# Optimization experiments

Measured on AMD Instinct MI355X. Metric: run time of the kernel, lower is better.

The kernel has to match this reference:

```python
import jax, jax.numpy as jnp
import numpy as np

N = 524288          # batch size
NUM_SD = 64         # socio-demographic chars
H = 128             # hidden size of TasteParams MLP
NUM_ALT_FEAT = 9    # alternative features
NUM_CLASSES = 3
# utility_structure: class k -> (start, end) column slice of x
SEGMENTS = [(0, 3), (3, 6), (6, 9)]


def setup_inputs() -> dict:
    key = jax.random.key(0)
    ks = jax.random.split(key, 8)
    s = 0.05
    return {
        "x": jax.random.normal(ks[0], (N, NUM_ALT_FEAT), jnp.float32),
        "z": jax.random.normal(ks[1], (N, NUM_SD), jnp.float32),
        "W1": jax.random.normal(ks[2], (NUM_SD, H), jnp.float32) * s,
        "b1": jax.random.normal(ks[3], (H,), jnp.float32) * s,
        "W2": jax.random.normal(ks[4], (H, H), jnp.float32) * s,
        "b2": jax.random.normal(ks[5], (H,), jnp.float32) * s,
        "W3": jax.random.normal(ks[6], (H, NUM_ALT_FEAT + NUM_CLASSES), jnp.float32) * s,
        "b3": jax.random.normal(ks[7], (NUM_ALT_FEAT + NUM_CLASSES,), jnp.float32) * s,
    }


def _forward(x, z, W1, b1, W2, b2, W3, b3):
    # TasteParams MLP: Linear-ReLU-Linear-ReLU-Linear
    h = jax.nn.relu(z @ W1 + b1)
    h = jax.nn.relu(h @ W2 + b2)
    b = h @ W3 + b3                        # (N, 12)
    # monotonic_constraints (num_classes==3, func_intercept=True)
    b = jnp.concatenate([
        -jax.nn.relu(-b[:, :6]),
        b[:, 6:7],
        -jax.nn.relu(-b[:, 7:9]),
        b[:, -NUM_CLASSES:],
    ], axis=1)
    taste = b[:, :NUM_ALT_FEAT]            # (N, 9)
    intercept = b[:, -NUM_CLASSES:]        # (N, 3)
    # MNL_layer with b: per-segment elementwise mult + reduce into logits column
    prod = x * taste                       # (N, 9)
    logits = jnp.stack(
        [prod[:, lo:hi].sum(axis=1) for (lo, hi) in SEGMENTS], axis=1
    )                                      # (N, 3)
    return logits + intercept


def reference(x, z, W1, b1, W2, b2, W3, b3):
    return _forward(x, z, W1, b1, W2, b2, W3, b3)
```

## Files before the change

kernel.cpp:

```cpp
#include <hip/hip_runtime.h>
#include <hip/hip_bf16.h>


typedef __bf16 bf16x8 __attribute__((ext_vector_type(8)));
typedef float  f32x16 __attribute__((ext_vector_type(16)));
typedef unsigned int uint2v __attribute__((ext_vector_type(2)));
typedef unsigned int uint4v __attribute__((ext_vector_type(4)));

#define MFMA32(a, b, c) __builtin_amdgcn_mfma_f32_32x32x16_bf16((a), (b), (c), 0, 0, 0)
#define PIN_AGPR(v) asm("" : "+a"(v))

#define SW3 0
#define SW1 1536
#define SW2 9728
#define SB1 26112
#define SB2 26240
#define SB3 26368
#define ZS_BYTE 52768
#define SMEM_ELTS (26384 + 32768)

#define NBLK    256
#define NTHR    512
#define NTILE   16384
#define WSTRIDE (NBLK * 8)

typedef __attribute__((address_space(3))) unsigned int lds_u32;
typedef __attribute__((address_space(1))) const unsigned int glb_u32;

__device__ __forceinline__ void gll16(const float* g, const void* l) {
  __builtin_amdgcn_global_load_lds((glb_u32*)g, (lds_u32*)l, 16, 0, 0);
}

__device__ __forceinline__ unsigned pkbf(float lo, float hi) {
  unsigned short lb = __builtin_bit_cast(unsigned short, (__bf16)lo);
  unsigned short hb = __builtin_bit_cast(unsigned short, (__bf16)hi);
  return ((unsigned)hb << 16) | (unsigned)lb;
}

template <int SUB>
__device__ __forceinline__ bf16x8 mk_bfrag(const f32x16 h) {
  constexpr int B = SUB * 8;
  unsigned p01 = pkbf(h[B + 0], h[B + 1]);
  unsigned p23 = pkbf(h[B + 2], h[B + 3]);
  unsigned p45 = pkbf(h[B + 4], h[B + 5]);
  unsigned p67 = pkbf(h[B + 6], h[B + 7]);
  unsigned d0, d1, d2, d3;
#if __has_builtin(__builtin_amdgcn_permlane32_swap)
  uint2v r1 = __builtin_amdgcn_permlane32_swap(p01, p45, false, false);
  uint2v r2 = __builtin_amdgcn_permlane32_swap(p23, p67, false, false);
  d0 = r1[0]; d2 = r1[1];
  d1 = r2[0]; d3 = r2[1];
#else
  int hi = (threadIdx.x >> 5) & 1;
  unsigned sp01 = (unsigned)__shfl_xor((int)p01, 32, 64);
  unsigned sp23 = (unsigned)__shfl_xor((int)p23, 32, 64);
  unsigned sp45 = (unsigned)__shfl_xor((int)p45, 32, 64);
  unsigned sp67 = (unsigned)__shfl_xor((int)p67, 32, 64);
  d0 = hi ? sp45 : p01;
  d2 = hi ? p45  : sp01;
  d1 = hi ? sp67 : p23;
  d3 = hi ? p67  : sp23;
#endif
  uint4v t; t[0] = d0; t[1] = d1; t[2] = d2; t[3] = d3;
  return __builtin_bit_cast(bf16x8, t);
}

__device__ __forceinline__ bf16x8 ldw(const __bf16* sm, int vaddr, int imm) {
  return *(const bf16x8*)((const char*)sm + vaddr + imm);
}

__device__ __forceinline__ float4 ldz(const __bf16* sm, int vaddr) {
  return *(const float4*)((const char*)sm + vaddr);
}

__device__ __forceinline__ bf16x8 biasA(__bf16 v) {
  bf16x8 f;
  #pragma unroll
  for (int i = 0; i < 8; ++i) f[i] = (__bf16)0.0f;
  f[0] = v;
  return f;
}

__global__ __launch_bounds__(512, 2)
void tastenet_kernel(const float* __restrict__ x, const float* __restrict__ z,
                     const float* __restrict__ W1, const float* __restrict__ b1,
                     const float* __restrict__ W2, const float* __restrict__ b2,
                     const float* __restrict__ W3, const float* __restrict__ b3,
                     float* __restrict__ out) {
  __shared__ __align__(16) __bf16 sm[SMEM_ELTS];
  const int tid = threadIdx.x;
  unsigned* smw = (unsigned*)sm;

  for (int i = tid; i < 4096; i += NTHR) {
    int m = i & 127, k = (i >> 7) * 2;
    smw[SW1 / 2 + m * 32 + (((k >> 3) ^ (m & 7)) << 2) + ((k >> 1) & 3)] =
        pkbf(W1[k * 128 + m], W1[(k + 1) * 128 + m]);
  }
  for (int i = tid; i < 8192; i += NTHR) {
    int m = i & 127, k = (i >> 7) * 2;
    smw[SW2 / 2 + m * 64 + (((k >> 3) ^ (m & 7)) << 2) + ((k >> 1) & 3)] =
        pkbf(W2[k * 128 + m], W2[(k + 1) * 128 + m]);
  }
  for (int i = tid; i < 768; i += NTHR) {
    int kk = i / 12, m = i - kk * 12, k = kk * 2;
    smw[SW3 / 2 + m * 64 + (((k >> 3) ^ (m & 7)) << 2) + ((k >> 1) & 3)] =
        pkbf(W3[k * 12 + m], W3[(k + 1) * 12 + m]);
  }
  if (tid < 128) { sm[SB1 + tid] = (__bf16)b1[tid]; sm[SB2 + tid] = (__bf16)b2[tid]; }
  if (tid < 12)  sm[SB3 + tid] = (__bf16)b3[tid];
  __syncthreads();

  const int wave = tid >> 6;
  const int lane = tid & 63;
  const int q    = lane >> 5;
  const int n    = lane & 31;
  const int s8   = n & 7;
  const int eq   = q ^ (s8 & 1);
  const int sh   = s8 >> 1;

  int aw1[4], aw2[4];
  #pragma unroll
  for (int j = 0; j < 4; ++j) {
    aw1[j] = n * 128 + eq * 16 + 32 * (j ^ sh);
    aw2[j] = n * 256 + eq * 16 + 32 * (j ^ sh);
  }

  const char* slotp = (const char*)sm + ZS_BYTE + wave * 8192;
  const int lr = lane >> 4, lc = lane & 15;
  int gofs[8];
  #pragma unroll
  for (int i = 0; i < 8; ++i) {
    int r = 4 * i + lr;
    gofs[i] = r * 64 + ((lc ^ (r & 15)) << 2);
  }
  int zrd[8];
  #pragma unroll
  for (int kt = 0; kt < 4; ++kt)
    #pragma unroll
    for (int s = 0; s < 2; ++s)
      zrd[2 * kt + s] =
          ZS_BYTE + wave * 8192 + n * 256 + (((4 * kt + 2 * q + s) ^ (n & 15)) << 4);

  bf16x8 ones;
  #pragma unroll
  for (int i = 0; i < 8; ++i) ones[i] = (__bf16)0.0f;
  if (q == 0) ones[0] = (__bf16)1.0f;
  PIN_AGPR(ones);

  bf16x8 ba1[4], ba2[4], ba3;
  #pragma unroll
  for (int f = 0; f < 4; ++f) {
    ba1[f] = biasA((q == 0) ? sm[SB1 + f * 32 + n] : (__bf16)0.0f);
    ba2[f] = biasA((q == 0) ? sm[SB2 + f * 32 + n] : (__bf16)0.0f);
    PIN_AGPR(ba1[f]); PIN_AGPR(ba2[f]);
  }
  ba3 = biasA((q == 0 && n < 12) ? sm[SB3 + n] : (__bf16)0.0f);
  PIN_AGPR(ba3);

  f32x16 zeroC;
  #pragma unroll
  for (int i = 0; i < 16; ++i) zeroC[i] = 0.0f;
  PIN_AGPR(zeroC);

  const int wid = blockIdx.x * 8 + wave;

  {
    const float* zb = z + (long)wid * 2048;
    #pragma unroll
    for (int i = 0; i < 8; ++i) gll16(zb + gofs[i], slotp + (i << 10));
  }

  #pragma unroll 1
  for (int t = wid; t < NTILE; t += WSTRIDE) {
    const long row = (long)t * 32 + n;

    asm volatile("s_waitcnt vmcnt(0)" ::: "memory");

    const float* xr = x + row * 9;
    float xv0 = xr[q * 4 + 0], xv1 = xr[q * 4 + 1];
    float xv2 = xr[q * 4 + 2], xv3 = xr[q * 4 + 3];
    float xv4 = xr[8];

    bf16x8 bz[4];
    #pragma unroll
    for (int kt = 0; kt < 4; ++kt) {
      float4 a = ldz(sm, zrd[2 * kt]);
      float4 b = ldz(sm, zrd[2 * kt + 1]);
      bf16x8 f;
      f[0] = (__bf16)a.x; f[1] = (__bf16)a.y; f[2] = (__bf16)a.z; f[3] = (__bf16)a.w;
      f[4] = (__bf16)b.x; f[5] = (__bf16)b.y; f[6] = (__bf16)b.z; f[7] = (__bf16)b.w;
      bz[kt] = f;
    }
    __builtin_amdgcn_sched_barrier(0);

    if (t + WSTRIDE < NTILE) {
      const float* zb = z + (long)(t + WSTRIDE) * 2048;
      #pragma unroll
      for (int i = 0; i < 8; ++i) gll16(zb + gofs[i], slotp + (i << 10));
    }
    __builtin_amdgcn_sched_barrier(0);

    bf16x8 bf2[8];
    #pragma unroll
    for (int fp = 0; fp < 2; ++fp) {
      f32x16 aA = MFMA32(ba1[2 * fp + 0], ones, zeroC);
      f32x16 aB = MFMA32(ba1[2 * fp + 1], ones, zeroC);
      PIN_AGPR(aA); PIN_AGPR(aB);
      #pragma unroll
      for (int kt = 0; kt < 4; ++kt) {
        aA = MFMA32(ldw(sm, aw1[kt], SW1 * 2 + (2 * fp + 0) * 4096), bz[kt], aA);
        aB = MFMA32(ldw(sm, aw1[kt], SW1 * 2 + (2 * fp + 1) * 4096), bz[kt], aB);
      }
      #pragma unroll
      for (int i = 0; i < 16; ++i) { aA[i] = fmaxf(aA[i], 0.0f); aB[i] = fmaxf(aB[i], 0.0f); }
      bf2[4 * fp + 0] = mk_bfrag<0>(aA);
      bf2[4 * fp + 1] = mk_bfrag<1>(aA);
      bf2[4 * fp + 2] = mk_bfrag<0>(aB);
      bf2[4 * fp + 3] = mk_bfrag<1>(aB);
    }

    f32x16 acc3 = MFMA32(ba3, ones, zeroC);
    PIN_AGPR(acc3);
    #pragma unroll
    for (int fp = 0; fp < 2; ++fp) {
      f32x16 aA = MFMA32(ba2[2 * fp + 0], ones, zeroC);
      f32x16 aB = MFMA32(ba2[2 * fp + 1], ones, zeroC);
      PIN_AGPR(aA); PIN_AGPR(aB);
      #pragma unroll
      for (int kt = 0; kt < 8; ++kt) {
        aA = MFMA32(ldw(sm, aw2[kt & 3], SW2 * 2 + (2 * fp + 0) * 8192 + 128 * (kt >> 2)),
                    bf2[kt], aA);
        aB = MFMA32(ldw(sm, aw2[kt & 3], SW2 * 2 + (2 * fp + 1) * 8192 + 128 * (kt >> 2)),
                    bf2[kt], aB);
      }
      #pragma unroll
      for (int i = 0; i < 16; ++i) { aA[i] = fmaxf(aA[i], 0.0f); aB[i] = fmaxf(aB[i], 0.0f); }
      acc3 = MFMA32(ldw(sm, aw2[0], SW3 * 2 + 128 * fp), mk_bfrag<0>(aA), acc3);
      acc3 = MFMA32(ldw(sm, aw2[1], SW3 * 2 + 128 * fp), mk_bfrag<1>(aA), acc3);
      acc3 = MFMA32(ldw(sm, aw2[2], SW3 * 2 + 128 * fp), mk_bfrag<0>(aB), acc3);
      acc3 = MFMA32(ldw(sm, aw2[3], SW3 * 2 + 128 * fp), mk_bfrag<1>(aB), acc3);
    }

    float t0 = acc3[0], t1 = acc3[1], t2 = acc3[2], t3 = acc3[3];
    float t4 = acc3[4], t5 = acc3[5], t6 = acc3[6], t7 = acc3[7];
    float o0 = 0.f, o1 = 0.f, o2 = 0.f, g1v = 0.f, g2v = 0.f;
    if (q == 0) {
      t0 = fminf(t0, 0.0f); t1 = fminf(t1, 0.0f);
      t2 = fminf(t2, 0.0f); t3 = fminf(t3, 0.0f);
      t4 = fminf(t4, 0.0f);
      o0 = xv0 * t0 + xv1 * t1 + xv2 * t2 + t5;
      o1 = xv3 * t3 + t6;
      o2 = xv4 * t4 + t7;
    } else {
      t0 = fminf(t0, 0.0f); t1 = fminf(t1, 0.0f);
      t3 = fminf(t3, 0.0f);
      g1v = xv0 * t0 + xv1 * t1;
      g2v = xv2 * t2 + xv3 * t3;
    }
    float a1v = __shfl_xor(g1v, 32, 64);
    float a2v = __shfl_xor(g2v, 32, 64);
    if (q == 0) {
      float* op = out + row * 3;
      op[0] = o0;
      op[1] = o1 + a1v;
      op[2] = o2 + a2v;
    }
  }
}

extern "C" void kernel_launch(void* const* d_in, const int* in_sizes, int n_in,
                              void* d_out, int out_size, void* d_ws, size_t ws_size,
                              hipStream_t stream) {
  const float* x  = (const float*)d_in[0];
  const float* z  = (const float*)d_in[1];
  const float* W1 = (const float*)d_in[2];
  const float* b1 = (const float*)d_in[3];
  const float* W2 = (const float*)d_in[4];
  const float* b2 = (const float*)d_in[5];
  const float* W3 = (const float*)d_in[6];
  const float* b3 = (const float*)d_in[7];
  tastenet_kernel<<<dim3(NBLK), dim3(NTHR), 0, stream>>>(
      x, z, W1, b1, W2, b2, W3, b3, (float*)d_out);
}
```

Before: 241.1 us.

## Split each tile across a wave pair with register-resident weight fragments

```diff
diff --git a/kernel.cpp b/kernel.cpp
--- a/kernel.cpp
+++ b/kernel.cpp
@@ -16,13 +16,16 @@
 #define SB1 26112
 #define SB2 26240
 #define SB3 26368
-#define ZS_BYTE 52768
-#define SMEM_ELTS (26384 + 32768)
-
-#define NBLK    256
-#define NTHR    512
-#define NTILE   16384
-#define WSTRIDE (NBLK * 8)
+#define SMEM_ELTS 26384
+
+#define ZSL(team)  ((team) * 8192)
+#define H1X(team)  (16384 + (team) * 8192)
+#define A3X(team)  (32768 + (team) * 2048)
+
+#define NBLK 512
+#define NTHR 256
+#define NTILE 16384
+#define TSTRIDE (NBLK * 2)
 
 typedef __attribute__((address_space(3))) unsigned int lds_u32;
 typedef __attribute__((address_space(1))) const unsigned int glb_u32;
@@ -68,7 +71,6 @@
 __device__ __forceinline__ bf16x8 ldw(const __bf16* sm, int vaddr, int imm) {
   return *(const bf16x8*)((const char*)sm + vaddr + imm);
 }
-
 __device__ __forceinline__ float4 ldz(const __bf16* sm, int vaddr) {
   return *(const float4*)((const char*)sm + vaddr);
 }
@@ -81,7 +83,7 @@
   return f;
 }
 
-__global__ __launch_bounds__(512, 2)
+__global__ __launch_bounds__(256, 2)
 void tastenet_kernel(const float* __restrict__ x, const float* __restrict__ z,
                      const float* __restrict__ W1, const float* __restrict__ b1,
                      const float* __restrict__ W2, const float* __restrict__ b2,
@@ -90,6 +92,7 @@
   __shared__ __align__(16) __bf16 sm[SMEM_ELTS];
   const int tid = threadIdx.x;
   unsigned* smw = (unsigned*)sm;
+  char* smb = (char*)sm;
 
   for (int i = tid; i < 4096; i += NTHR) {
     int m = i & 127, k = (i >> 7) * 2;
@@ -117,15 +120,62 @@
   const int s8   = n & 7;
   const int eq   = q ^ (s8 & 1);
   const int sh   = s8 >> 1;
-
-  int aw1[4], aw2[4];
+  const int half = wave & 1;
+  const int team = wave >> 1;
+
+  int aw1v[4], aw2v[4];
   #pragma unroll
   for (int j = 0; j < 4; ++j) {
-    aw1[j] = n * 128 + eq * 16 + 32 * (j ^ sh);
-    aw2[j] = n * 256 + eq * 16 + 32 * (j ^ sh);
-  }
-
-  const char* slotp = (const char*)sm + ZS_BYTE + wave * 8192;
+    aw1v[j] = n * 128 + eq * 16 + 32 * (j ^ sh);
+    aw2v[j] = n * 256 + eq * 16 + 32 * (j ^ sh);
+  }
+
+  bf16x8 w1f[8], w2f[16], w3f[4];
+  #pragma unroll
+  for (int b = 0; b < 2; ++b)
+    #pragma unroll
+    for (int kt = 0; kt < 4; ++kt) {
+      w1f[b * 4 + kt] = ldw(sm, aw1v[kt] + (2 * half + b) * 4096, SW1 * 2);
+      PIN_AGPR(w1f[b * 4 + kt]);
+    }
+  #pragma unroll
+  for (int b = 0; b < 2; ++b)
+    #pragma unroll
+    for (int kt = 0; kt < 8; ++kt) {
+      w2f[b * 8 + kt] =
+          ldw(sm, aw2v[kt & 3] + (2 * half + b) * 8192 + 128 * (kt >> 2), SW2 * 2);
+      PIN_AGPR(w2f[b * 8 + kt]);
+    }
+  #pragma unroll
+  for (int kt = 0; kt < 4; ++kt) {
+    w3f[kt] = ldw(sm, aw2v[kt] + 128 * half, SW3 * 2);
+    PIN_AGPR(w3f[kt]);
+  }
+
+  bf16x8 ones;
+  #pragma unroll
+  for (int i = 0; i < 8; ++i) ones[i] = (__bf16)0.0f;
+  if (q == 0) ones[0] = (__bf16)1.0f;
+  PIN_AGPR(ones);
+
+  bf16x8 ba1[2], ba2[2], ba3;
+  #pragma unroll
+  for (int b = 0; b < 2; ++b) {
+    ba1[b] = biasA((q == 0) ? sm[SB1 + (2 * half + b) * 32 + n] : (__bf16)0.0f);
+    ba2[b] = biasA((q == 0) ? sm[SB2 + (2 * half + b) * 32 + n] : (__bf16)0.0f);
+    PIN_AGPR(ba1[b]); PIN_AGPR(ba2[b]);
+  }
+  ba3 = biasA((half == 1 && q == 0 && n < 12) ? sm[SB3 + n] : (__bf16)0.0f);
+  PIN_AGPR(ba3);
+
+  f32x16 zeroC;
+  #pragma unroll
+  for (int i = 0; i < 16; ++i) zeroC[i] = 0.0f;
+  PIN_AGPR(zeroC);
+
+  __syncthreads();
+
+  const char* slotp = smb + ZSL(team);
   const int lr = lane >> 4, lc = lane & 15;
   int gofs[8];
   #pragma unroll
@@ -139,47 +189,29 @@
     #pragma unroll
     for (int s = 0; s < 2; ++s)
       zrd[2 * kt + s] =
-          ZS_BYTE + wave * 8192 + n * 256 + (((4 * kt + 2 * q + s) ^ (n & 15)) << 4);
-
-  bf16x8 ones;
-  #pragma unroll
-  for (int i = 0; i < 8; ++i) ones[i] = (__bf16)0.0f;
-  if (q == 0) ones[0] = (__bf16)1.0f;
-  PIN_AGPR(ones);
-
-  bf16x8 ba1[4], ba2[4], ba3;
-  #pragma unroll
-  for (int f = 0; f < 4; ++f) {
-    ba1[f] = biasA((q == 0) ? sm[SB1 + f * 32 + n] : (__bf16)0.0f);
-    ba2[f] = biasA((q == 0) ? sm[SB2 + f * 32 + n] : (__bf16)0.0f);
-    PIN_AGPR(ba1[f]); PIN_AGPR(ba2[f]);
-  }
-  ba3 = biasA((q == 0 && n < 12) ? sm[SB3 + n] : (__bf16)0.0f);
-  PIN_AGPR(ba3);
-
-  f32x16 zeroC;
-  #pragma unroll
-  for (int i = 0; i < 16; ++i) zeroC[i] = 0.0f;
-  PIN_AGPR(zeroC);
-
-  const int wid = blockIdx.x * 8 + wave;
-
-  {
-    const float* zb = z + (long)wid * 2048;
+          ZSL(team) + n * 256 + (((4 * kt + 2 * q + s) ^ (n & 15)) << 4);
+
+  const int teamg = blockIdx.x * 2 + team;
+
+  if (!half) {
+    const float* zb = z + (long)teamg * 2048;
     #pragma unroll
     for (int i = 0; i < 8; ++i) gll16(zb + gofs[i], slotp + (i << 10));
-  }
+    asm volatile("s_waitcnt vmcnt(0)" ::: "memory");
+  }
+  __syncthreads();
 
   #pragma unroll 1
-  for (int t = wid; t < NTILE; t += WSTRIDE) {
+  for (int t = teamg; t < NTILE; t += TSTRIDE) {
     const long row = (long)t * 32 + n;
 
-    asm volatile("s_waitcnt vmcnt(0)" ::: "memory");
-
-    const float* xr = x + row * 9;
-    float xv0 = xr[q * 4 + 0], xv1 = xr[q * 4 + 1];
-    float xv2 = xr[q * 4 + 2], xv3 = xr[q * 4 + 3];
-    float xv4 = xr[8];
+    float xv0 = 0.f, xv1 = 0.f, xv2 = 0.f, xv3 = 0.f, xv4 = 0.f;
+    if (half) {
+      const float* xr = x + row * 9;
+      xv0 = xr[q * 4 + 0]; xv1 = xr[q * 4 + 1];
+      xv2 = xr[q * 4 + 2]; xv3 = xr[q * 4 + 3];
+      xv4 = xr[8];
+    }
 
     bf16x8 bz[4];
     #pragma unroll
@@ -191,79 +223,103 @@
       f[4] = (__bf16)b.x; f[5] = (__bf16)b.y; f[6] = (__bf16)b.z; f[7] = (__bf16)b.w;
       bz[kt] = f;
     }
-    __builtin_amdgcn_sched_barrier(0);
-
-    if (t + WSTRIDE < NTILE) {
-      const float* zb = z + (long)(t + WSTRIDE) * 2048;
+
+    f32x16 dA = MFMA32(ba1[0], ones, zeroC);
+    f32x16 dB = MFMA32(ba1[1], ones, zeroC);
+    PIN_AGPR(dA); PIN_AGPR(dB);
+    #pragma unroll
+    for (int kt = 0; kt < 4; ++kt) {
+      dA = MFMA32(w1f[kt],     bz[kt], dA);
+      dB = MFMA32(w1f[4 + kt], bz[kt], dB);
+    }
+    #pragma unroll
+    for (int i = 0; i < 16; ++i) { dA[i] = fmaxf(dA[i], 0.0f); dB[i] = fmaxf(dB[i], 0.0f); }
+    bf16x8 f0 = mk_bfrag<0>(dA), f1 = mk_bfrag<1>(dA);
+    bf16x8 f2 = mk_bfrag<0>(dB), f3 = mk_bfrag<1>(dB);
+
+    {
+      char* hb = smb + H1X(team) + half * 4096 + lane * 16;
+      *(bf16x8*)(hb + 0)    = f0;
+      *(bf16x8*)(hb + 1024) = f1;
+      *(bf16x8*)(hb + 2048) = f2;
+      *(bf16x8*)(hb + 3072) = f3;
+    }
+    __syncthreads();
+
+    if (!half && t + TSTRIDE < NTILE) {
+      const float* zb = z + (long)(t + TSTRIDE) * 2048;
       #pragma unroll
       for (int i = 0; i < 8; ++i) gll16(zb + gofs[i], slotp + (i << 10));
     }
-    __builtin_amdgcn_sched_barrier(0);
 
     bf16x8 bf2[8];
-    #pragma unroll
-    for (int fp = 0; fp < 2; ++fp) {
-      f32x16 aA = MFMA32(ba1[2 * fp + 0], ones, zeroC);
-      f32x16 aB = MFMA32(ba1[2 * fp + 1], ones, zeroC);
-      PIN_AGPR(aA); PIN_AGPR(aB);
-      #pragma unroll
-      for (int kt = 0; kt < 4; ++kt) {
-        aA = MFMA32(ldw(sm, aw1[kt], SW1 * 2 + (2 * fp + 0) * 4096), bz[kt], aA);
-        aB = MFMA32(ldw(sm, aw1[kt], SW1 * 2 + (2 * fp + 1) * 4096), bz[kt], aB);
+    bf2[4 * half + 0] = f0; bf2[4 * half + 1] = f1;
+    bf2[4 * half + 2] = f2; bf2[4 * half + 3] = f3;
+    {
+      const char* hr = smb + H1X(team) + (half ^ 1) * 4096 + lane * 16;
+      bf2[4 * (half ^ 1) + 0] = *(const bf16x8*)(hr + 0);
+      bf2[4 * (half ^ 1) + 1] = *(const bf16x8*)(hr + 1024);
+      bf2[4 * (half ^ 1) + 2] = *(const bf16x8*)(hr + 2048);
+      bf2[4 * (half ^ 1) + 3] = *(const bf16x8*)(hr + 3072);
+    }
+
+    f32x16 pA = MFMA32(ba2[0], ones, zeroC);
+    f32x16 pB = MFMA32(ba2[1], ones, zeroC);
+    PIN_AGPR(pA); PIN_AGPR(pB);
+    #pragma unroll
+    for (int kt = 0; kt < 8; ++kt) {
+      pA = MFMA32(w2f[kt],     bf2[kt], pA);
+      pB = MFMA32(w2f[8 + kt], bf2[kt], pB);
+    }
+    #pragma unroll
+    for (int i = 0; i < 16; ++i) { pA[i] = fmaxf(pA[i], 0.0f); pB[i] = fmaxf(pB[i], 0.0f); }
+
+    f32x16 a3 = MFMA32(ba3, ones, zeroC);
+    PIN_AGPR(a3);
+    a3 = MFMA32(w3f[0], mk_bfrag<0>(pA), a3);
+    a3 = MFMA32(w3f[1], mk_bfrag<1>(pA), a3);
+    a3 = MFMA32(w3f[2], mk_bfrag<0>(pB), a3);
+    a3 = MFMA32(w3f[3], mk_bfrag<1>(pB), a3);
+
+    if (!half) {
+      float4 w0, w1v;
+      w0.x = a3[0]; w0.y = a3[1]; w0.z = a3[2]; w0.w = a3[3];
+      w1v.x = a3[4]; w1v.y = a3[5]; w1v.z = a3[6]; w1v.w = a3[7];
+      *(float4*)(smb + A3X(team) + lane * 16) = w0;
+      *(float4*)(smb + A3X(team) + 1024 + lane * 16) = w1v;
+      asm volatile("s_waitcnt vmcnt(0)" ::: "memory");
+    }
+    __syncthreads();
+
+    if (half) {
+      float4 p0 = *(const float4*)(smb + A3X(team) + lane * 16);
+      float4 p1 = *(const float4*)(smb + A3X(team) + 1024 + lane * 16);
+      float t0 = a3[0] + p0.x, t1 = a3[1] + p0.y;
+      float t2 = a3[2] + p0.z, t3 = a3[3] + p0.w;
+      float t4 = a3[4] + p1.x, t5 = a3[5] + p1.y;
+      float t6 = a3[6] + p1.z, t7 = a3[7] + p1.w;
+      float o0 = 0.f, o1 = 0.f, o2 = 0.f, g1v = 0.f, g2v = 0.f;
+      if (q == 0) {
+        t0 = fminf(t0, 0.0f); t1 = fminf(t1, 0.0f);
+        t2 = fminf(t2, 0.0f); t3 = fminf(t3, 0.0f);
+        t4 = fminf(t4, 0.0f);
+        o0 = xv0 * t0 + xv1 * t1 + xv2 * t2 + t5;
+        o1 = xv3 * t3 + t6;
+        o2 = xv4 * t4 + t7;
+      } else {
+        t0 = fminf(t0, 0.0f); t1 = fminf(t1, 0.0f);
+        t3 = fminf(t3, 0.0f);
+        g1v = xv0 * t0 + xv1 * t1;
+        g2v = xv2 * t2 + xv3 * t3;
       }
-      #pragma unroll
-      for (int i = 0; i < 16; ++i) { aA[i] = fmaxf(aA[i], 0.0f); aB[i] = fmaxf(aB[i], 0.0f); }
-      bf2[4 * fp + 0] = mk_bfrag<0>(aA);
-      bf2[4 * fp + 1] = mk_bfrag<1>(aA);
-      bf2[4 * fp + 2] = mk_bfrag<0>(aB);
-      bf2[4 * fp + 3] = mk_bfrag<1>(aB);
-    }
-
-    f32x16 acc3 = MFMA32(ba3, ones, zeroC);
-    PIN_AGPR(acc3);
-    #pragma unroll
-    for (int fp = 0; fp < 2; ++fp) {
-      f32x16 aA = MFMA32(ba2[2 * fp + 0], ones, zeroC);
-      f32x16 aB = MFMA32(ba2[2 * fp + 1], ones, zeroC);
-      PIN_AGPR(aA); PIN_AGPR(aB);
-      #pragma unroll
-      for (int kt = 0; kt < 8; ++kt) {
-        aA = MFMA32(ldw(sm, aw2[kt & 3], SW2 * 2 + (2 * fp + 0) * 8192 + 128 * (kt >> 2)),
-                    bf2[kt], aA);
-        aB = MFMA32(ldw(sm, aw2[kt & 3], SW2 * 2 + (2 * fp + 1) * 8192 + 128 * (kt >> 2)),
-                    bf2[kt], aB);
+      float a1v = __shfl_xor(g1v, 32, 64);
+      float a2v = __shfl_xor(g2v, 32, 64);
+      if (q == 0) {
+        float* op = out + row * 3;
+        op[0] = o0;
+        op[1] = o1 + a1v;
+        op[2] = o2 + a2v;
       }
-      #pragma unroll
-      for (int i = 0; i < 16; ++i) { aA[i] = fmaxf(aA[i], 0.0f); aB[i] = fmaxf(aB[i], 0.0f); }
-      acc3 = MFMA32(ldw(sm, aw2[0], SW3 * 2 + 128 * fp), mk_bfrag<0>(aA), acc3);
-      acc3 = MFMA32(ldw(sm, aw2[1], SW3 * 2 + 128 * fp), mk_bfrag<1>(aA), acc3);
-      acc3 = MFMA32(ldw(sm, aw2[2], SW3 * 2 + 128 * fp), mk_bfrag<0>(aB), acc3);
-      acc3 = MFMA32(ldw(sm, aw2[3], SW3 * 2 + 128 * fp), mk_bfrag<1>(aB), acc3);
-    }
-
-    float t0 = acc3[0], t1 = acc3[1], t2 = acc3[2], t3 = acc3[3];
-    float t4 = acc3[4], t5 = acc3[5], t6 = acc3[6], t7 = acc3[7];
-    float o0 = 0.f, o1 = 0.f, o2 = 0.f, g1v = 0.f, g2v = 0.f;
-    if (q == 0) {
-      t0 = fminf(t0, 0.0f); t1 = fminf(t1, 0.0f);
-      t2 = fminf(t2, 0.0f); t3 = fminf(t3, 0.0f);
-      t4 = fminf(t4, 0.0f);
-      o0 = xv0 * t0 + xv1 * t1 + xv2 * t2 + t5;
-      o1 = xv3 * t3 + t6;
-      o2 = xv4 * t4 + t7;
-    } else {
-      t0 = fminf(t0, 0.0f); t1 = fminf(t1, 0.0f);
-      t3 = fminf(t3, 0.0f);
-      g1v = xv0 * t0 + xv1 * t1;
-      g2v = xv2 * t2 + xv3 * t3;
-    }
-    float a1v = __shfl_xor(g1v, 32, 64);
-    float a2v = __shfl_xor(g2v, 32, 64);
-    if (q == 0) {
-      float* op = out + row * 3;
-      op[0] = o0;
-      op[1] = o1 + a1v;
-      op[2] = o2 + a2v;
     }
   }
 }
```

After: 823.2 us. 3.41x slower.
